# Optimization experiments

Measured on AMD Instinct MI355X. Metric: run time of the kernel, lower is better.

## Reference

```python
import jax, jax.numpy as jnp
import numpy as np

H = 256  # hidden size (hard-coded in the torch module)


def gru_bidir(x, Wi_f, Wh_f, bi_f, bh_f, Wi_b, Wh_b, bi_b, bh_b):
    """Bidirectional single-layer GRU, PyTorch gate order (r,z,n), h0=0.
    x: [B,T,E] -> [B,T,2H]."""
    def run(x_tbe, Wi, Wh, bi, bh):
        xp = x_tbe @ Wi.T + bi  # precompute input projections: [T,B,3H]
        def step(h, xpt):
            hp = h @ Wh.T + bh
            r = jax.nn.sigmoid(xpt[:, :H] + hp[:, :H])
            z = jax.nn.sigmoid(xpt[:, H:2 * H] + hp[:, H:2 * H])
            n = jnp.tanh(xpt[:, 2 * H:] + r * hp[:, 2 * H:])
            h_new = (1.0 - z) * n + z * h
            return h_new, h_new
        h0 = jnp.zeros((x_tbe.shape[1], H), x_tbe.dtype)
        return jax.lax.scan(step, h0, xp)[1]
    x_tbe = jnp.swapaxes(x, 0, 1)  # time-major for scan
    fwd = run(x_tbe, Wi_f, Wh_f, bi_f, bh_f)
    bwd = run(x_tbe[::-1], Wi_b, Wh_b, bi_b, bh_b)[::-1]
    return jnp.swapaxes(jnp.concatenate([fwd, bwd], axis=-1), 0, 1)


def setup_inputs():
    key = jax.random.key(0)
    ks = jax.random.split(key, 23)
    B, LC, LO, NOPT, E = 16, 128, 64, 5, 300
    s = 1.0 / np.sqrt(H)
    p = lambda k, shp: jax.random.uniform(k, shp, jnp.float32, -s, s)
    return {
        "context": jax.random.normal(ks[0], (B, LC, E), jnp.float32),
        "context_lens": jax.random.randint(ks[1], (B,), 1, LC + 1).astype(jnp.int32),
        "options": jax.random.normal(ks[2], (B, NOPT, LO, E), jnp.float32),
        "option_lens": jax.random.randint(ks[3], (B, NOPT), 1, LO + 1).astype(jnp.int32),
        "rnn_Wi_f": p(ks[4], (3 * H, E)), "rnn_Wh_f": p(ks[5], (3 * H, H)),
        "rnn_bi_f": p(ks[6], (3 * H,)), "rnn_bh_f": p(ks[7], (3 * H,)),
        "rnn_Wi_b": p(ks[8], (3 * H, E)), "rnn_Wh_b": p(ks[9], (3 * H, H)),
        "rnn_bi_b": p(ks[10], (3 * H,)), "rnn_bh_b": p(ks[11], (3 * H,)),
        "att_Wi_f": p(ks[12], (3 * H, H)), "att_Wh_f": p(ks[13], (3 * H, H)),
        "att_bi_f": p(ks[14], (3 * H,)), "att_bh_f": p(ks[15], (3 * H,)),
        "att_Wi_b": p(ks[16], (3 * H, H)), "att_Wh_b": p(ks[17], (3 * H, H)),
        "att_bi_b": p(ks[18], (3 * H,)), "att_bh_b": p(ks[19], (3 * H,)),
        "Wk": p(ks[20], (H, 2 * H)), "Wq": p(ks[21], (H, 2 * H)),
        "v_energy": p(ks[22], (H,)),
    }


def reference(context, context_lens, options, option_lens,
              rnn_Wi_f, rnn_Wh_f, rnn_bi_f, rnn_bh_f,
              rnn_Wi_b, rnn_Wh_b, rnn_bi_b, rnn_bh_b,
              att_Wi_f, att_Wh_f, att_bi_f, att_bh_f,
              att_Wi_b, att_Wh_b, att_bi_b, att_bh_b,
              Wk, Wq, v_energy):
    # NOTE: context_lens / option_lens are accepted but unused, exactly as in the torch forward.
    rnn_p = (rnn_Wi_f, rnn_Wh_f, rnn_bi_f, rnn_bh_f, rnn_Wi_b, rnn_Wh_b, rnn_bi_b, rnn_bh_b)
    att_p = (att_Wi_f, att_Wh_f, att_bi_f, att_bh_f, att_Wi_b, att_Wh_b, att_bi_b, att_bh_b)
    ctx_key = gru_bidir(context, *rnn_p) @ Wk.T  # [B,LC,H]
    opts = jnp.swapaxes(options, 0, 1)  # [NOPT,B,LO,E] (matches options.transpose(1,0) loop)
    eps = 1e-8

    def one_option(carry, option):
        opt_q = gru_bidir(option, *rnn_p) @ Wq.T  # [B,LO,H]
        # Bahdanau additive energies: [B,LO,LC]
        e = jnp.einsum('bqch,h->bqc',
                       jnp.tanh(opt_q[:, :, None, :] + ctx_key[:, None, :, :]),
                       v_energy)
        # softmax over option dim, aggregate option queries per context step: [B,LC,H]
        a_ctx = jnp.einsum('bqc,bqh->bch', jax.nn.softmax(e, axis=1), opt_q)
        # softmax over context dim, aggregate context keys per option step: [B,LO,H]
        a_opt = jnp.einsum('bqc,bch->bqh', jax.nn.softmax(e, axis=2), ctx_key)
        m_ctx = gru_bidir(a_ctx, *att_p).mean(axis=1)  # [B,2H]
        m_opt = gru_bidir(a_opt, *att_p).mean(axis=1)  # [B,2H]
        na = jnp.maximum(jnp.linalg.norm(m_ctx, axis=1), eps)
        nb = jnp.maximum(jnp.linalg.norm(m_opt, axis=1), eps)
        return carry, jnp.sum(m_ctx * m_opt, axis=1) / (na * nb)

    _, logits = jax.lax.scan(one_option, None, opts)  # [NOPT,B]
    return jax.nn.softmax(logits.T, axis=1)  # [B,NOPT]
```

## Files before the change

kernel.cpp:

```cpp
#include <hip/hip_runtime.h>
#include <cstdint>
#include <cstddef>

#define LOG2E 1.4426950408889634f

using f32x4 = __attribute__((ext_vector_type(4))) float;
using s16x8 = __attribute__((ext_vector_type(8))) short;
using s16x4 = __attribute__((ext_vector_type(4))) short;

__device__ __forceinline__ short f2bf(float f){
  unsigned u = __builtin_bit_cast(unsigned, f);
  u = u + 0x7FFFu + ((u >> 16) & 1u);
  return (short)(u >> 16);
}
__device__ __forceinline__ float bf2f(short s){
  unsigned u = ((unsigned)(unsigned short)s) << 16;
  return __builtin_bit_cast(float, u);
}
__device__ __forceinline__ float fexp2(float x){ return __builtin_amdgcn_exp2f(x); }
__device__ __forceinline__ float frcp (float x){ return __builtin_amdgcn_rcpf(x); }
__device__ __forceinline__ float sigmoid_f(float x){
  x = fminf(fmaxf(x, -30.f), 30.f);
  return frcp(1.f + fexp2(-LOG2E * x));
}
__device__ __forceinline__ float tanh_f(float x){
  x = fminf(fmaxf(x, -15.f), 15.f);
  float e = fexp2(2.f * LOG2E * x);
  return (e - 1.f) * frcp(e + 1.f);
}

__global__ __launch_bounds__(256) void gemm_k(
    const float* __restrict__ A, const float* __restrict__ W,
    const float* __restrict__ bias, void* __restrict__ Cout,
    int M, int N, int K, int outBf16)
{
  __shared__ short As[64*40];
  __shared__ short Ws[64*40];
  const int tid  = threadIdx.x;
  const int lane = tid & 63;
  const int wave = tid >> 6;
  const int wm   = wave >> 1, wn = wave & 1;
  const int c    = lane & 15, rg = lane >> 4;
  const int bm   = blockIdx.y * 64, bn = blockIdx.x * 64;
  const int K4   = K >> 2;
  const int nkt  = (K + 31) >> 5;
  f32x4 acc[2][2] = {};
  for (int kt = 0; kt < nkt; ++kt){
    #pragma unroll
    for (int h = 0; h < 2; ++h){
      int idx = tid + h*256;
      int row = idx >> 3, q = idx & 7;
      int kq  = kt*8 + q;
      f32x4 av = {0.f,0.f,0.f,0.f}, wv4 = {0.f,0.f,0.f,0.f};
      if (kq < K4){
        av  = *(const f32x4*)(A + (size_t)(bm+row)*K + (size_t)kq*4);
        wv4 = *(const f32x4*)(W + (size_t)(bn+row)*K + (size_t)kq*4);
      }
      s16x4 ap, wp;
      #pragma unroll
      for (int i = 0; i < 4; ++i){ ap[i] = f2bf(av[i]); wp[i] = f2bf(wv4[i]); }
      *(s16x4*)&As[row*40 + q*4] = ap;
      *(s16x4*)&Ws[row*40 + q*4] = wp;
    }
    __syncthreads();
    s16x8 af[2], bf[2];
    #pragma unroll
    for (int mi = 0; mi < 2; ++mi) af[mi] = *(const s16x8*)&As[(wm*32 + mi*16 + c)*40 + rg*8];
    #pragma unroll
    for (int ni = 0; ni < 2; ++ni) bf[ni] = *(const s16x8*)&Ws[(wn*32 + ni*16 + c)*40 + rg*8];
    #pragma unroll
    for (int mi = 0; mi < 2; ++mi)
      #pragma unroll
      for (int ni = 0; ni < 2; ++ni)
        acc[mi][ni] = __builtin_amdgcn_mfma_f32_16x16x32_bf16(af[mi], bf[ni], acc[mi][ni], 0, 0, 0);
    __syncthreads();
  }
  #pragma unroll
  for (int mi = 0; mi < 2; ++mi)
    #pragma unroll
    for (int ni = 0; ni < 2; ++ni)
      #pragma unroll
      for (int i = 0; i < 4; ++i){
        int row = bm + wm*32 + mi*16 + rg*4 + i;
        int col = bn + wn*32 + ni*16 + c;
        float v = acc[mi][ni][i] + (bias ? bias[col] : 0.f);
        if (outBf16) ((short*)Cout)[(size_t)row*N + col] = f2bf(v);
        else         ((float*)Cout)[(size_t)row*N + col] = v;
      }
}

__global__ __launch_bounds__(512) void gru_scan_k(
    int nA, int TA, int sBA, int bMA,
    const short* __restrict__ xpfA, const short* __restrict__ xpbA, float* __restrict__ outA,
    int TB, int sBB, int bMB,
    const short* __restrict__ xpfB, const short* __restrict__ xpbB, float* __restrict__ outB,
    const float* __restrict__ Whf, const float* __restrict__ Whb,
    const float* __restrict__ bhf, const float* __restrict__ bhb)
{
  __shared__ short h_bf[16*256];
  __shared__ short xp_s[16*768];
  __shared__ float bh_s[768];

  const int tid  = threadIdx.x;
  const int w    = tid >> 6;
  const int lane = tid & 63;
  const int c    = lane & 15;
  const int rg   = lane >> 4;

  int T, strideB, baseRow, dir;
  const short* xp; float* outp;
  const float* Wh; const float* bh;
  {
    int bid = blockIdx.x;
    if (bid < nA){
      int idx = bid >> 1; dir = bid & 1;
      T = TA; strideB = sBA; baseRow = idx * bMA;
      xp = dir ? xpbA : xpfA; outp = outA;
    } else {
      int jj = bid - nA; int idx = jj >> 1; dir = jj & 1;
      T = TB; strideB = sBB; baseRow = idx * bMB;
      xp = dir ? xpbB : xpfB; outp = outB;
    }
    Wh = dir ? Whb : Whf;
    bh = dir ? bhb : bhf;
  }

  #pragma unroll
  for (int i = 0; i < 8; ++i) h_bf[tid*8 + i] = 0;
  for (int i = tid; i < 768; i += 512) bh_s[i] = bh[i];

  s16x8 wfrag[6][8];
  #pragma unroll
  for (int s = 0; s < 6; ++s){
    const float* wr = Wh + (size_t)((w + 8*s)*16 + c)*256 + rg*8;
    #pragma unroll
    for (int kb = 0; kb < 8; ++kb){
      f32x4 lo = *(const f32x4*)(wr + kb*32);
      f32x4 hi = *(const f32x4*)(wr + kb*32 + 4);
      s16x8 f;
      #pragma unroll
      for (int i = 0; i < 4; ++i){ f[i] = f2bf(lo[i]); f[4+i] = f2bf(hi[i]); }
      wfrag[s][kb] = f;
    }
  }
  float hprev[2][4] = {};
  const f32x4 fzero = {0.f, 0.f, 0.f, 0.f};
  __syncthreads();

  for (int t = 0; t < T; ++t){
    const int tt = dir ? (T - 1 - t) : t;
    #pragma unroll
    for (int i2 = 0; i2 < 3; ++i2){
      int idx8 = tid + 512*i2;
      int row  = idx8 / 96;
      int u    = idx8 - row*96;
      const short* src = xp + (size_t)(baseRow + row*strideB + tt)*768 + u*8;
      __builtin_amdgcn_global_load_lds((const __attribute__((address_space(1))) void*)src,
                                       (__attribute__((address_space(3))) void*)&xp_s[idx8*8],
                                       16, 0, 0);
    }
    f32x4 acc[6];
    #pragma unroll
    for (int s = 0; s < 6; ++s) acc[s] = fzero;
    #pragma unroll
    for (int kb = 0; kb < 8; ++kb){
      const int k0 = kb*32 + rg*8;
      const s16x8 a = *(const s16x8*)&h_bf[c*256 + (k0 ^ ((c & 7) << 3))];
      #pragma unroll
      for (int s = 0; s < 6; ++s)
        acc[s] = __builtin_amdgcn_mfma_f32_16x16x32_bf16(a, wfrag[s][kb], acc[s], 0, 0, 0);
    }
    __syncthreads();
    #pragma unroll
    for (int g = 0; g < 2; ++g){
      const int j = (w + 8*g)*16 + c;
      const float bhr = bh_s[j], bhz = bh_s[256 + j], bhn = bh_s[512 + j];
      #pragma unroll
      for (int i = 0; i < 4; ++i){
        const int b = rg*4 + i;
        const float xr = bf2f(xp_s[b*768 + j]);
        const float xz = bf2f(xp_s[b*768 + 256 + j]);
        const float xn = bf2f(xp_s[b*768 + 512 + j]);
        float r  = sigmoid_f(acc[g][i]   + bhr + xr);
        float z  = sigmoid_f(acc[2+g][i] + bhz + xz);
        float nn = tanh_f(xn + r*(acc[4+g][i] + bhn));
        float hnew = (1.f - z)*nn + z*hprev[g][i];
        hprev[g][i] = hnew;
        h_bf[b*256 + (j ^ ((b & 7) << 3))] = f2bf(hnew);
        outp[(size_t)(baseRow + b*strideB + tt)*512 + (size_t)dir*256 + j] = hnew;
      }
    }
    __syncthreads();
  }
}

__global__ __launch_bounds__(256) void energy_k(
    const float* __restrict__ oq, const float* __restrict__ ck,
    const float* __restrict__ v, float* __restrict__ e)
{
  __shared__ float oqs[4][256];
  __shared__ float vs[256];
  const int bid = blockIdx.x;
  const int o  = bid >> 8;
  const int b  = (bid >> 4) & 15;
  const int qg = bid & 15;
  const int tid = threadIdx.x;
  const int wv = tid >> 6, lane = tid & 63;
  const int q = qg*4 + wv;
  vs[tid] = v[tid];
  const float* oqrow = oq + (size_t)((b*5 + o)*64 + q)*256;
  #pragma unroll
  for (int i = 0; i < 4; ++i) oqs[wv][lane + i*64] = oqrow[lane + i*64];
  __syncthreads();
  float acc0 = 0.f, acc1 = 0.f;
  const float* ckb = ck + (size_t)b*128*256;
  for (int h = 0; h < 256; ++h){
    float t  = oqs[wv][h];
    float vh = vs[h];
    acc0 += tanh_f(t + ckb[(size_t)lane*256 + h]) * vh;
    acc1 += tanh_f(t + ckb[(size_t)(lane+64)*256 + h]) * vh;
  }
  const size_t ebase = (size_t)((o*16 + b)*64 + q)*128;
  e[ebase + lane]      = acc0;
  e[ebase + lane + 64] = acc1;
}

__global__ __launch_bounds__(256) void actx_k(
    const float* __restrict__ e, const float* __restrict__ oq, float* __restrict__ a_ctx)
{
  __shared__ float wq[64];
  const int bid = blockIdx.x;
  const int o  = bid >> 11;
  const int b  = (bid >> 7) & 15;
  const int cc = bid & 127;
  const int tid = threadIdx.x;
  if (tid < 64){
    float x = e[((size_t)((o*16 + b)*64 + tid))*128 + cc];
    float mx = x;
    #pragma unroll
    for (int off = 32; off; off >>= 1) mx = fmaxf(mx, __shfl_xor(mx, off));
    float p = fexp2((x - mx)*LOG2E);
    float sm = p;
    #pragma unroll
    for (int off = 32; off; off >>= 1) sm += __shfl_xor(sm, off);
    wq[tid] = p * frcp(sm);
  }
  __syncthreads();
  float acc = 0.f;
  const float* oqb = oq + ((size_t)(b*320 + o*64))*256 + tid;
  #pragma unroll 4
  for (int q = 0; q < 64; ++q) acc += wq[q] * oqb[(size_t)q*256];
  a_ctx[((size_t)((o*16 + b)*128 + cc))*256 + tid] = acc;
}

__global__ __launch_bounds__(256) void aopt_k(
    const float* __restrict__ e, const float* __restrict__ ck, float* __restrict__ a_opt)
{
  __shared__ float wc[128];
  __shared__ float red[4];
  const int bid = blockIdx.x;
  const int o = bid >> 10;
  const int b = (bid >> 6) & 15;
  const int q = bid & 63;
  const int tid = threadIdx.x, lane = tid & 63, wv = tid >> 6;
  const float* er = e + ((size_t)((o*16 + b)*64 + q))*128;
  float x = (tid < 128) ? er[tid] : -3.0e38f;
  float mx = x;
  #pragma unroll
  for (int off = 32; off; off >>= 1) mx = fmaxf(mx, __shfl_xor(mx, off));
  if (lane == 0 && wv < 2) red[wv] = mx;
  __syncthreads();
  float gm = fmaxf(red[0], red[1]);
  float p = (tid < 128) ? fexp2((x - gm)*LOG2E) : 0.f;
  float sm = p;
  #pragma unroll
  for (int off = 32; off; off >>= 1) sm += __shfl_xor(sm, off);
  if (lane == 0 && wv < 2) red[2 + wv] = sm;
  __syncthreads();
  float tot = red[2] + red[3];
  if (tid < 128) wc[tid] = p * frcp(tot);
  __syncthreads();
  float acc = 0.f;
  const float* ckb = ck + (size_t)b*128*256 + tid;
  #pragma unroll 4
  for (int cc = 0; cc < 128; ++cc) acc += wc[cc] * ckb[(size_t)cc*256];
  a_opt[((size_t)((o*16 + b)*64 + q))*256 + tid] = acc;
}

__global__ __launch_bounds__(512) void mean_k(
    const float* __restrict__ src, float* __restrict__ dst, int T)
{
  const int r = blockIdx.x;
  const int f = threadIdx.x;
  const float* s = src + (size_t)r*T*512 + f;
  float acc = 0.f;
  for (int t = 0; t < T; ++t) acc += s[(size_t)t*512];
  dst[(size_t)r*512 + f] = acc / (float)T;
}

__global__ __launch_bounds__(512) void final_k(
    const float* __restrict__ mc, const float* __restrict__ mo, float* __restrict__ out)
{
  __shared__ float lg[80];
  const int tid = threadIdx.x;
  const int wv = tid >> 6, lane = tid & 63;
  #pragma unroll
  for (int it = 0; it < 10; ++it){
    const int p = wv + it*8;
    const float* a = mc + (size_t)p*512;
    const float* b = mo + (size_t)p*512;
    float d = 0.f, na = 0.f, nb = 0.f;
    #pragma unroll
    for (int i = 0; i < 8; ++i){
      float x = a[lane + 64*i], y = b[lane + 64*i];
      d += x*y; na += x*x; nb += y*y;
    }
    #pragma unroll
    for (int off = 32; off; off >>= 1){
      d += __shfl_xor(d, off); na += __shfl_xor(na, off); nb += __shfl_xor(nb, off);
    }
    if (lane == 0){
      float den = fmaxf(sqrtf(na), 1e-8f) * fmaxf(sqrtf(nb), 1e-8f);
      lg[p] = d / den;
    }
  }
  __syncthreads();
  if (tid < 16){
    float l[5];
    float mx = -3.0e38f;
    #pragma unroll
    for (int o = 0; o < 5; ++o){ l[o] = lg[o*16 + tid]; mx = fmaxf(mx, l[o]); }
    float s = 0.f;
    #pragma unroll
    for (int o = 0; o < 5; ++o){ l[o] = fexp2((l[o]-mx)*LOG2E); s += l[o]; }
    #pragma unroll
    for (int o = 0; o < 5; ++o) out[tid*5 + o] = l[o] / s;
  }
}

static constexpr size_t OFF_XP_CTX_F  = 0;
static constexpr size_t OFF_XP_CTX_B  = 3145728;
static constexpr size_t OFF_XP_OPT_F  = 6291456;
static constexpr size_t OFF_XP_OPT_B  = 14155776;
static constexpr size_t OFF_AXP_CTX_F = 0;
static constexpr size_t OFF_AXP_CTX_B = 15728640;
static constexpr size_t OFF_AXP_OPT_F = 31457280;
static constexpr size_t OFF_AXP_OPT_B = 39321600;
static constexpr size_t REGION_B      = 47185920;
static constexpr size_t OFF_CTX_ENC   = REGION_B;
static constexpr size_t OFF_OPT_ENC   = REGION_B + 4194304;
static constexpr size_t OFF_ATT_ENC_C = REGION_B;
static constexpr size_t OFF_ATT_ENC_O = REGION_B + 20971520;
static constexpr size_t OFF_CTX_KEY   = 78643200;
static constexpr size_t OFF_OPT_Q     = 80740352;
static constexpr size_t OFF_E         = 85983232;
static constexpr size_t OFF_ACTX      = 88604672;
static constexpr size_t OFF_AOPT      = 99090432;
static constexpr size_t OFF_MCTX      = 104333312;
static constexpr size_t OFF_MOPT      = 104497152;
static constexpr size_t WS_NEED       = 104660992;

extern "C" void kernel_launch(void* const* d_in, const int* in_sizes, int n_in,
                              void* d_out, int out_size, void* d_ws, size_t ws_size,
                              hipStream_t stream)
{
  (void)in_sizes; (void)n_in; (void)out_size;
  if (ws_size < WS_NEED) return;

  const float* context = (const float*)d_in[0];
  const float* options = (const float*)d_in[2];
  const float* rWi_f = (const float*)d_in[4];
  const float* rWh_f = (const float*)d_in[5];
  const float* rbi_f = (const float*)d_in[6];
  const float* rbh_f = (const float*)d_in[7];
  const float* rWi_b = (const float*)d_in[8];
  const float* rWh_b = (const float*)d_in[9];
  const float* rbi_b = (const float*)d_in[10];
  const float* rbh_b = (const float*)d_in[11];
  const float* aWi_f = (const float*)d_in[12];
  const float* aWh_f = (const float*)d_in[13];
  const float* abi_f = (const float*)d_in[14];
  const float* abh_f = (const float*)d_in[15];
  const float* aWi_b = (const float*)d_in[16];
  const float* aWh_b = (const float*)d_in[17];
  const float* abi_b = (const float*)d_in[18];
  const float* abh_b = (const float*)d_in[19];
  const float* Wk    = (const float*)d_in[20];
  const float* Wq    = (const float*)d_in[21];
  const float* vE    = (const float*)d_in[22];

  char* ws = (char*)d_ws;
  short* xp_ctx_f  = (short*)(ws + OFF_XP_CTX_F);
  short* xp_ctx_b  = (short*)(ws + OFF_XP_CTX_B);
  short* xp_opt_f  = (short*)(ws + OFF_XP_OPT_F);
  short* xp_opt_b  = (short*)(ws + OFF_XP_OPT_B);
  short* axp_ctx_f = (short*)(ws + OFF_AXP_CTX_F);
  short* axp_ctx_b = (short*)(ws + OFF_AXP_CTX_B);
  short* axp_opt_f = (short*)(ws + OFF_AXP_OPT_F);
  short* axp_opt_b = (short*)(ws + OFF_AXP_OPT_B);
  float* ctx_enc   = (float*)(ws + OFF_CTX_ENC);
  float* opt_enc   = (float*)(ws + OFF_OPT_ENC);
  float* att_enc_c = (float*)(ws + OFF_ATT_ENC_C);
  float* att_enc_o = (float*)(ws + OFF_ATT_ENC_O);
  float* ctx_key   = (float*)(ws + OFF_CTX_KEY);
  float* opt_q     = (float*)(ws + OFF_OPT_Q);
  float* e_all     = (float*)(ws + OFF_E);
  float* a_ctx     = (float*)(ws + OFF_ACTX);
  float* a_opt     = (float*)(ws + OFF_AOPT);
  float* m_ctx     = (float*)(ws + OFF_MCTX);
  float* m_opt     = (float*)(ws + OFF_MOPT);

  dim3 blk256(256), blk512(512);

  gemm_k<<<dim3(12, 32), blk256, 0, stream>>>(context, rWi_f, rbi_f, xp_ctx_f, 2048, 768, 300, 1);
  gemm_k<<<dim3(12, 32), blk256, 0, stream>>>(context, rWi_b, rbi_b, xp_ctx_b, 2048, 768, 300, 1);
  gemm_k<<<dim3(12, 80), blk256, 0, stream>>>(options, rWi_f, rbi_f, xp_opt_f, 5120, 768, 300, 1);
  gemm_k<<<dim3(12, 80), blk256, 0, stream>>>(options, rWi_b, rbi_b, xp_opt_b, 5120, 768, 300, 1);
  gru_scan_k<<<12, blk512, 0, stream>>>(2, 128, 128, 0, xp_ctx_f, xp_ctx_b, ctx_enc,
                                        64, 320, 64, xp_opt_f, xp_opt_b, opt_enc,
                                        rWh_f, rWh_b, rbh_f, rbh_b);
  gemm_k<<<dim3(4, 32), blk256, 0, stream>>>(ctx_enc, Wk, nullptr, ctx_key, 2048, 256, 512, 0);
  gemm_k<<<dim3(4, 80), blk256, 0, stream>>>(opt_enc, Wq, nullptr, opt_q, 5120, 256, 512, 0);
  energy_k<<<1280, blk256, 0, stream>>>(opt_q, ctx_key, vE, e_all);
  actx_k<<<10240, blk256, 0, stream>>>(e_all, opt_q, a_ctx);
  aopt_k<<<5120, blk256, 0, stream>>>(e_all, ctx_key, a_opt);
  gemm_k<<<dim3(12, 160), blk256, 0, stream>>>(a_ctx, aWi_f, abi_f, axp_ctx_f, 10240, 768, 256, 1);
  gemm_k<<<dim3(12, 160), blk256, 0, stream>>>(a_ctx, aWi_b, abi_b, axp_ctx_b, 10240, 768, 256, 1);
  gemm_k<<<dim3(12, 80),  blk256, 0, stream>>>(a_opt, aWi_f, abi_f, axp_opt_f, 5120, 768, 256, 1);
  gemm_k<<<dim3(12, 80),  blk256, 0, stream>>>(a_opt, aWi_b, abi_b, axp_opt_b, 5120, 768, 256, 1);
  gru_scan_k<<<20, blk512, 0, stream>>>(10, 128, 128, 2048, axp_ctx_f, axp_ctx_b, att_enc_c,
                                        64, 64, 1024, axp_opt_f, axp_opt_b, att_enc_o,
                                        aWh_f, aWh_b, abh_f, abh_b);
  mean_k<<<80, blk512, 0, stream>>>(att_enc_c, m_ctx, 128);
  mean_k<<<80, blk512, 0, stream>>>(att_enc_o, m_opt, 64);
  final_k<<<1, blk512, 0, stream>>>(m_ctx, m_opt, (float*)d_out);
}
```

Baseline: 1.500 ms.

## Double-buffer GRU input projections and fold hidden bias into MFMA accumulators

The GRU scan kernel now prefetches the next timestep's input projections into a second LDS buffer while the current step computes. The hidden bias is kept in registers and used as the initial MFMA accumulator value, and the work is reorganised per gate group so each group's gate math follows its own MFMAs. Sigmoid and tanh drop their clamps and tanh uses a single reciprocal, which relies on exp2/rcp saturating correctly for large inputs. Launch bounds now request two blocks per CU, which may constrain register use for the 48 weight fragments held per thread.

```diff
diff --git a/kernel.cpp b/kernel.cpp
--- a/kernel.cpp
+++ b/kernel.cpp
@@ -20,14 +20,13 @@
 __device__ __forceinline__ float fexp2(float x){ return __builtin_amdgcn_exp2f(x); }
 __device__ __forceinline__ float frcp (float x){ return __builtin_amdgcn_rcpf(x); }
 __device__ __forceinline__ float sigmoid_f(float x){
-  x = fminf(fmaxf(x, -30.f), 30.f);
   return frcp(1.f + fexp2(-LOG2E * x));
 }
 __device__ __forceinline__ float tanh_f(float x){
-  x = fminf(fmaxf(x, -15.f), 15.f);
-  float e = fexp2(2.f * LOG2E * x);
-  return (e - 1.f) * frcp(e + 1.f);
-}
+  return 1.f - 2.f * frcp(fexp2(2.f * LOG2E * x) + 1.f);
+}
+
+#define MFMA16(a,b,c) __builtin_amdgcn_mfma_f32_16x16x32_bf16(a,b,c,0,0,0)
 
 __global__ __launch_bounds__(256) void gemm_k(
     const float* __restrict__ A, const float* __restrict__ W,
@@ -72,7 +71,7 @@
     for (int mi = 0; mi < 2; ++mi)
       #pragma unroll
       for (int ni = 0; ni < 2; ++ni)
-        acc[mi][ni] = __builtin_amdgcn_mfma_f32_16x16x32_bf16(af[mi], bf[ni], acc[mi][ni], 0, 0, 0);
+        acc[mi][ni] = MFMA16(af[mi], bf[ni], acc[mi][ni]);
     __syncthreads();
   }
   #pragma unroll
@@ -89,7 +88,7 @@
       }
 }
 
-__global__ __launch_bounds__(512) void gru_scan_k(
+__global__ __launch_bounds__(512, 2) void gru_scan_k(
     int nA, int TA, int sBA, int bMA,
     const short* __restrict__ xpfA, const short* __restrict__ xpbA, float* __restrict__ outA,
     int TB, int sBB, int bMB,
@@ -98,8 +97,7 @@
     const float* __restrict__ bhf, const float* __restrict__ bhb)
 {
   __shared__ short h_bf[16*256];
-  __shared__ short xp_s[16*768];
-  __shared__ float bh_s[768];
+  __shared__ short xp_s[2][16*768];
 
   const int tid  = threadIdx.x;
   const int w    = tid >> 6;
@@ -127,67 +125,90 @@
 
   #pragma unroll
   for (int i = 0; i < 8; ++i) h_bf[tid*8 + i] = 0;
-  for (int i = tid; i < 768; i += 512) bh_s[i] = bh[i];
-
-  s16x8 wfrag[6][8];
-  #pragma unroll
-  for (int s = 0; s < 6; ++s){
-    const float* wr = Wh + (size_t)((w + 8*s)*16 + c)*256 + rg*8;
-    #pragma unroll
-    for (int kb = 0; kb < 8; ++kb){
-      f32x4 lo = *(const f32x4*)(wr + kb*32);
-      f32x4 hi = *(const f32x4*)(wr + kb*32 + 4);
-      s16x8 f;
-      #pragma unroll
-      for (int i = 0; i < 4; ++i){ f[i] = f2bf(lo[i]); f[4+i] = f2bf(hi[i]); }
-      wfrag[s][kb] = f;
-    }
-  }
-  float hprev[2][4] = {};
-  const f32x4 fzero = {0.f, 0.f, 0.f, 0.f};
-  __syncthreads();
-
-  for (int t = 0; t < T; ++t){
-    const int tt = dir ? (T - 1 - t) : t;
+
+  float bhc[2][3];
+  #pragma unroll
+  for (int g = 0; g < 2; ++g){
+    const int j = (w + 8*g)*16 + c;
+    bhc[g][0] = bh[j]; bhc[g][1] = bh[256 + j]; bhc[g][2] = bh[512 + j];
+  }
+
+  s16x8 wfrag[2][3][8];
+  #pragma unroll
+  for (int g = 0; g < 2; ++g)
+    #pragma unroll
+    for (int gate = 0; gate < 3; ++gate){
+      const float* wr = Wh + (size_t)(gate*256 + (w + 8*g)*16 + c)*256 + rg*8;
+      #pragma unroll
+      for (int kb = 0; kb < 8; ++kb){
+        f32x4 lo = *(const f32x4*)(wr + kb*32);
+        f32x4 hi = *(const f32x4*)(wr + kb*32 + 4);
+        s16x8 f;
+        #pragma unroll
+        for (int i = 0; i < 4; ++i){ f[i] = f2bf(lo[i]); f[4+i] = f2bf(hi[i]); }
+        wfrag[g][gate][kb] = f;
+      }
+    }
+
+  auto stage = [&](int tt_, int buf){
     #pragma unroll
     for (int i2 = 0; i2 < 3; ++i2){
       int idx8 = tid + 512*i2;
       int row  = idx8 / 96;
       int u    = idx8 - row*96;
-      const short* src = xp + (size_t)(baseRow + row*strideB + tt)*768 + u*8;
+      const short* src = xp + (size_t)(baseRow + row*strideB + tt_)*768 + u*8;
       __builtin_amdgcn_global_load_lds((const __attribute__((address_space(1))) void*)src,
-                                       (__attribute__((address_space(3))) void*)&xp_s[idx8*8],
+                                       (__attribute__((address_space(3))) void*)&xp_s[buf][idx8*8],
                                        16, 0, 0);
     }
-    f32x4 acc[6];
-    #pragma unroll
-    for (int s = 0; s < 6; ++s) acc[s] = fzero;
-    #pragma unroll
-    for (int kb = 0; kb < 8; ++kb){
-      const int k0 = kb*32 + rg*8;
-      const s16x8 a = *(const s16x8*)&h_bf[c*256 + (k0 ^ ((c & 7) << 3))];
-      #pragma unroll
-      for (int s = 0; s < 6; ++s)
-        acc[s] = __builtin_amdgcn_mfma_f32_16x16x32_bf16(a, wfrag[s][kb], acc[s], 0, 0, 0);
-    }
-    __syncthreads();
+  };
+
+  float hprev[2][4] = {};
+  stage(dir ? (T - 1) : 0, 0);
+  __syncthreads();
+
+  for (int t = 0; t < T; ++t){
+    const int cur = t & 1;
+    if (t + 1 < T) stage(dir ? (T - 2 - t) : (t + 1), cur ^ 1);
+    const int tt = dir ? (T - 1 - t) : t;
+    float hnew[2][4];
     #pragma unroll
     for (int g = 0; g < 2; ++g){
       const int j = (w + 8*g)*16 + c;
-      const float bhr = bh_s[j], bhz = bh_s[256 + j], bhn = bh_s[512 + j];
+      f32x4 ar, az, an;
+      #pragma unroll
+      for (int i = 0; i < 4; ++i){ ar[i] = bhc[g][0]; az[i] = bhc[g][1]; an[i] = bhc[g][2]; }
+      #pragma unroll
+      for (int kb = 0; kb < 8; ++kb){
+        const int k0 = kb*32 + rg*8;
+        const s16x8 a = *(const s16x8*)&h_bf[c*256 + (k0 ^ ((c & 7) << 3))];
+        ar = MFMA16(a, wfrag[g][0][kb], ar);
+        az = MFMA16(a, wfrag[g][1][kb], az);
+        an = MFMA16(a, wfrag[g][2][kb], an);
+      }
+      const short* xrow = &xp_s[cur][0];
       #pragma unroll
       for (int i = 0; i < 4; ++i){
         const int b = rg*4 + i;
-        const float xr = bf2f(xp_s[b*768 + j]);
-        const float xz = bf2f(xp_s[b*768 + 256 + j]);
-        const float xn = bf2f(xp_s[b*768 + 512 + j]);
-        float r  = sigmoid_f(acc[g][i]   + bhr + xr);
-        float z  = sigmoid_f(acc[2+g][i] + bhz + xz);
-        float nn = tanh_f(xn + r*(acc[4+g][i] + bhn));
-        float hnew = (1.f - z)*nn + z*hprev[g][i];
-        hprev[g][i] = hnew;
-        h_bf[b*256 + (j ^ ((b & 7) << 3))] = f2bf(hnew);
-        outp[(size_t)(baseRow + b*strideB + tt)*512 + (size_t)dir*256 + j] = hnew;
+        const float xr = bf2f(xrow[b*768 + j]);
+        const float xz = bf2f(xrow[b*768 + 256 + j]);
+        const float xn = bf2f(xrow[b*768 + 512 + j]);
+        float r = sigmoid_f(ar[i] + xr);
+        float z = sigmoid_f(az[i] + xz);
+        float n = tanh_f(xn + r*an[i]);
+        float h = n + z*(hprev[g][i] - n);
+        hprev[g][i] = h; hnew[g][i] = h;
+        outp[(size_t)(baseRow + b*strideB + tt)*512 + (size_t)dir*256 + j] = h;
+      }
+    }
+    __syncthreads();
+    #pragma unroll
+    for (int g = 0; g < 2; ++g){
+      const int j = (w + 8*g)*16 + c;
+      #pragma unroll
+      for (int i = 0; i < 4; ++i){
+        const int b = rg*4 + i;
+        h_bf[b*256 + (j ^ ((b & 7) << 3))] = f2bf(hnew[g][i]);
       }
     }
     __syncthreads();
```

Result: slower. 1.663 ms (+10.9%).
